# Optimization experiments

Hardware: AMD Instinct MI355X
Metric: run time of the kernel (lower is better)

The kernel has to match this reference:

```python
import jax, jax.numpy as jnp
import numpy as np

B, N, E = 32, 2048, 768
OUT = 384
SPARSITY = 4
LOCAL_C = (E + SPARSITY - 1) // SPARSITY  # 192
HID = 16
LN_EPS = 1e-5


def _layernorm(x, w, b):
    mu = jnp.mean(x, axis=-1, keepdims=True)
    var = jnp.mean(jnp.square(x - mu), axis=-1, keepdims=True)
    return (x - mu) * jax.lax.rsqrt(var + LN_EPS) * w + b


def setup_inputs() -> dict:
    key = jax.random.key(0)
    ks = jax.random.split(key, 8)
    s = 0.02
    return {
        "x": jax.random.normal(ks[0], (B, N, E), dtype=jnp.float32),
        # global head: Linear(E,16) -> LN(16) -> GELU -> Linear(16,1)
        "w_g1": jax.random.normal(ks[1], (E, HID), dtype=jnp.float32) * s,
        "b_g1": jnp.zeros((HID,), dtype=jnp.float32),
        "ln_g_w": jnp.ones((HID,), dtype=jnp.float32),
        "ln_g_b": jnp.zeros((HID,), dtype=jnp.float32),
        "w_g2": jax.random.normal(ks[2], (HID, 1), dtype=jnp.float32) * s,
        "b_g2": jnp.zeros((1,), dtype=jnp.float32),
        # local head: Linear(192,384) -> LN(384) -> GELU
        "w_l": jax.random.normal(ks[3], (LOCAL_C, OUT), dtype=jnp.float32) * s,
        "b_l": jnp.zeros((OUT,), dtype=jnp.float32),
        "ln_l_w": jnp.ones((OUT,), dtype=jnp.float32),
        "ln_l_b": jnp.zeros((OUT,), dtype=jnp.float32),
    }


def reference(x, w_g1, b_g1, ln_g_w, ln_g_b, w_g2, b_g2, w_l, b_l, ln_l_w, ln_l_b):
    # local branch: strided gather -> Linear -> LN -> GELU  [B,N,OUT]
    local = x[..., ::SPARSITY]                                   # [B,N,192]
    local_feat = jax.nn.gelu(_layernorm(local @ w_l + b_l, ln_l_w, ln_l_b),
                             approximate=False)
    # global branch: Linear -> LN -> GELU -> Linear -> [B,N,1] (broadcasts)
    g = jax.nn.gelu(_layernorm(x @ w_g1 + b_g1, ln_g_w, ln_g_b),
                    approximate=False)
    global_feat = g @ w_g2 + b_g2                                # [B,N,1]
    # AdaptiveAvgPool1d(OUT) on last dim; E % OUT == 0 -> exact pairwise mean
    pooled = jnp.mean(x.reshape(B, N, OUT, E // OUT), axis=-1)   # [B,N,OUT]
    return global_feat + pooled + local_feat
```

## Files before the change

### kernel.cpp

```cpp
#include <hip/hip_runtime.h>
#include <hip/hip_bf16.h>

#define B_   32
#define N_   2048
#define E_   768
#define OUT_ 384
#define HID_ 16
constexpr int ROWS   = B_ * N_;
constexpr int TILE_M = 16;
constexpr int NT     = OUT_ / 16;
constexpr int KT_L   = 6;
constexpr int KT_G   = 24;
constexpr int S_AL   = 194;
constexpr int S_PL   = 392;

typedef __attribute__((ext_vector_type(8))) short bf16x8;
typedef __attribute__((ext_vector_type(4))) float f32x4;

__device__ __forceinline__ short f2bf(float f) {
  union { float f; unsigned u; } v; v.f = f;
  unsigned r = v.u + 0x7fffu + ((v.u >> 16) & 1u);
  return (short)(r >> 16);
}
__device__ __forceinline__ float bf2f(short s) {
  union { unsigned u; float f; } v; v.u = ((unsigned)(unsigned short)s) << 16;
  return v.f;
}

__device__ __forceinline__ float fast_erf(float x) {
  const float ax = __builtin_fabsf(x);
  const float t  = __builtin_amdgcn_rcpf(__builtin_fmaf(0.3275911f, ax, 1.0f));
  float p = __builtin_fmaf(1.061405429f, t, -1.453152027f);
  p = __builtin_fmaf(p, t, 1.421413741f);
  p = __builtin_fmaf(p, t, -0.284496736f);
  p = __builtin_fmaf(p, t, 0.254829592f);
  const float e = __expf(-ax * ax);
  const float y = __builtin_fmaf(-p * t, e, 1.0f);
  return __builtin_copysignf(y, x);
}
__device__ __forceinline__ float gelu(float v) {
  return 0.5f * v * (1.0f + fast_erf(v * 0.70710678118654752f));
}

__global__ void prep_kernel(const float* __restrict__ w_l, const float* __restrict__ w_g1,
                            short* __restrict__ wsL, short* __restrict__ wsG) {
  int t = blockIdx.x * blockDim.x + threadIdx.x;
  int wave = t >> 6, ln = t & 63;
  int kg = ln >> 4, c16 = ln & 15;
  if (wave < NT * KT_L) {
    int n = wave / KT_L, ks = wave % KT_L;
    bf16x8 v;
#pragma unroll
    for (int j = 0; j < 8; ++j) {
      int k = ks * 32 + kg * 8 + j;
      v[j] = f2bf(w_l[k * OUT_ + n * 16 + c16]);
    }
    *reinterpret_cast<bf16x8*>(&wsL[(size_t)(wave * 64 + ln) * 8]) = v;
  } else if (wave < NT * KT_L + KT_G) {
    int ks = wave - NT * KT_L;
    bf16x8 v;
#pragma unroll
    for (int j = 0; j < 8; ++j) {
      int k = ks * 32 + kg * 8 + j;
      v[j] = f2bf(w_g1[k * HID_ + c16]);
    }
    *reinterpret_cast<bf16x8*>(&wsG[(size_t)(ks * 64 + ln) * 8]) = v;
  }
}

template <bool USE_WS>
__global__ __launch_bounds__(128, 3)
void spectre_kernel(const float* __restrict__ x,
                    const float* __restrict__ w_g1, const float* __restrict__ b_g1,
                    const float* __restrict__ ln_g_w, const float* __restrict__ ln_g_b,
                    const float* __restrict__ w_g2, const float* __restrict__ b_g2,
                    const float* __restrict__ w_l, const float* __restrict__ b_l,
                    const float* __restrict__ ln_l_w, const float* __restrict__ ln_l_b,
                    const short* __restrict__ wsL, const short* __restrict__ wsG,
                    float* __restrict__ out) {
  __shared__ short al[TILE_M * S_AL];
  __shared__ short pl[TILE_M * S_PL];
  __shared__ float red2[2][16][17];
  __shared__ float reds[2][16][2];

  const int tid = threadIdx.x;
  const int wv  = tid >> 6;
  const int ln  = tid & 63;
  const int kg  = ln >> 4;
  const int l15 = ln & 15;
  const int row0 = blockIdx.x * TILE_M;

  const float* xb = x + (size_t)row0 * E_;

  f32x4 accg = {0.f, 0.f, 0.f, 0.f};
  {
    const float* pA = xb + l15 * E_ + kg * 8;
    float4 xu0[4], xu1[4];
    bf16x8 gb[4];
#pragma unroll
    for (int s = 0; s < 4; ++s) {
      const int ks = wv * 12 + s;
      xu0[s] = *reinterpret_cast<const float4*>(pA + ks * 32);
      xu1[s] = *reinterpret_cast<const float4*>(pA + ks * 32 + 4);
      if constexpr (USE_WS) {
        gb[s] = *reinterpret_cast<const bf16x8*>(&wsG[(ks * 64 + ln) * 8]);
      } else {
#pragma unroll
        for (int j = 0; j < 8; ++j) gb[s][j] = f2bf(w_g1[(ks * 32 + kg * 8 + j) * HID_ + l15]);
      }
    }
#pragma unroll
    for (int i = 0; i < 12; ++i) {
      const int s  = i & 3;
      const int ks = wv * 12 + i;
      const float4 u0 = xu0[s];
      const float4 u1 = xu1[s];
      const bf16x8 b  = gb[s];
      if (i + 4 < 12) {
        const int k2 = ks + 4;
        xu0[s] = *reinterpret_cast<const float4*>(pA + k2 * 32);
        xu1[s] = *reinterpret_cast<const float4*>(pA + k2 * 32 + 4);
        if constexpr (USE_WS) {
          gb[s] = *reinterpret_cast<const bf16x8*>(&wsG[(k2 * 64 + ln) * 8]);
        } else {
#pragma unroll
          for (int j = 0; j < 8; ++j) gb[s][j] = f2bf(w_g1[(k2 * 32 + kg * 8 + j) * HID_ + l15]);
        }
      }
      short2 lv;
      lv.x = f2bf(u0.x);
      lv.y = f2bf(u1.x);
      *reinterpret_cast<short2*>(&al[l15 * S_AL + 8 * ks + 2 * kg]) = lv;
      short4 pv;
      pv.x = f2bf(0.5f * (u0.x + u0.y));
      pv.y = f2bf(0.5f * (u0.z + u0.w));
      pv.z = f2bf(0.5f * (u1.x + u1.y));
      pv.w = f2bf(0.5f * (u1.z + u1.w));
      *reinterpret_cast<short4*>(&pl[l15 * S_PL + ks * 16 + kg * 4]) = pv;
      const bf16x8 a = { lv.x, f2bf(u0.y), f2bf(u0.z), f2bf(u0.w),
                         lv.y, f2bf(u1.y), f2bf(u1.z), f2bf(u1.w) };
      accg = __builtin_amdgcn_mfma_f32_16x16x32_bf16(a, b, accg, 0, 0, 0);
    }
  }
#pragma unroll
  for (int r = 0; r < 4; ++r) red2[wv][kg * 4 + r][l15] = accg[r];

  const float bg  = b_g1[l15];
  const float lgw = ln_g_w[l15];
  const float lgb = ln_g_b[l15];
  const float wg2 = w_g2[l15];
  const float bg2 = b_g2[0];
  float blv[12];
#pragma unroll
  for (int n = 0; n < 12; ++n) blv[n] = b_l[(wv * 12 + n) * 16 + l15];

  __syncthreads();

  f32x4 acc[12];
#pragma unroll
  for (int n = 0; n < 12; ++n) acc[n] = (f32x4){0.f, 0.f, 0.f, 0.f};

  bf16x8 bb[2][6];
#pragma unroll
  for (int j = 0; j < 6; ++j) {
    const int ng = wv * 12 + j;
    if constexpr (USE_WS) {
      bb[0][j] = *reinterpret_cast<const bf16x8*>(&wsL[((ng * KT_L + 0) * 64 + ln) * 8]);
    } else {
#pragma unroll
      for (int jj = 0; jj < 8; ++jj)
        bb[0][j][jj] = f2bf(w_l[(0 * 32 + kg * 8 + jj) * OUT_ + ng * 16 + l15]);
    }
  }
  bf16x8 aLc = *reinterpret_cast<const bf16x8*>(&al[l15 * S_AL + kg * 8]);
  bf16x8 aLn;
#pragma unroll
  for (int ks = 0; ks < KT_L; ++ks) {
#pragma unroll
    for (int j = 0; j < 6; ++j) {
      const int ng = wv * 12 + 6 + j;
      if constexpr (USE_WS) {
        bb[1][j] = *reinterpret_cast<const bf16x8*>(&wsL[((ng * KT_L + ks) * 64 + ln) * 8]);
      } else {
#pragma unroll
        for (int jj = 0; jj < 8; ++jj)
          bb[1][j][jj] = f2bf(w_l[(ks * 32 + kg * 8 + jj) * OUT_ + ng * 16 + l15]);
      }
    }
#pragma unroll
    for (int j = 0; j < 6; ++j)
      acc[j] = __builtin_amdgcn_mfma_f32_16x16x32_bf16(aLc, bb[0][j], acc[j], 0, 0, 0);
    if (ks < KT_L - 1) {
      aLn = *reinterpret_cast<const bf16x8*>(&al[l15 * S_AL + (ks + 1) * 32 + kg * 8]);
#pragma unroll
      for (int j = 0; j < 6; ++j) {
        const int ng = wv * 12 + j;
        if constexpr (USE_WS) {
          bb[0][j] = *reinterpret_cast<const bf16x8*>(&wsL[((ng * KT_L + ks + 1) * 64 + ln) * 8]);
        } else {
#pragma unroll
          for (int jj = 0; jj < 8; ++jj)
            bb[0][j][jj] = f2bf(w_l[((ks + 1) * 32 + kg * 8 + jj) * OUT_ + ng * 16 + l15]);
        }
      }
    }
#pragma unroll
    for (int j = 0; j < 6; ++j)
      acc[6 + j] = __builtin_amdgcn_mfma_f32_16x16x32_bf16(aLc, bb[1][j], acc[6 + j], 0, 0, 0);
    if (ks < KT_L - 1) aLc = aLn;
  }

  float s1[4] = {0.f, 0.f, 0.f, 0.f}, s2[4] = {0.f, 0.f, 0.f, 0.f};
#pragma unroll
  for (int n = 0; n < 12; ++n) {
#pragma unroll
    for (int r = 0; r < 4; ++r) {
      const float v = acc[n][r] + blv[n];
      acc[n][r] = v;
      s1[r] += v;
      s2[r] += v * v;
    }
  }
#pragma unroll
  for (int m = 1; m < 16; m <<= 1) {
#pragma unroll
    for (int r = 0; r < 4; ++r) {
      s1[r] += __shfl_xor(s1[r], m);
      s2[r] += __shfl_xor(s2[r], m);
    }
  }
  if (l15 == 0) {
#pragma unroll
    for (int r = 0; r < 4; ++r) {
      reds[wv][kg * 4 + r][0] = s1[r];
      reds[wv][kg * 4 + r][1] = s2[r];
    }
  }
  __syncthreads();

  float lwv[12], lbv[12];
#pragma unroll
  for (int n = 0; n < 12; ++n) {
    const int col = (wv * 12 + n) * 16 + l15;
    lwv[n] = ln_l_w[col];
    lbv[n] = ln_l_b[col];
  }

  float gf[4];
#pragma unroll
  for (int r = 0; r < 4; ++r) {
    const int row = kg * 4 + r;
    const float y = red2[0][row][l15] + red2[1][row][l15] + bg;
    float s = y, q = y * y;
#pragma unroll
    for (int m = 1; m < 16; m <<= 1) {
      s += __shfl_xor(s, m);
      q += __shfl_xor(q, m);
    }
    const float mean = s * (1.f / 16.f);
    const float var  = q * (1.f / 16.f) - mean * mean;
    const float rstd = rsqrtf(var + 1e-5f);
    const float vn = (y - mean) * rstd * lgw + lgb;
    float ps = gelu(vn) * wg2;
#pragma unroll
    for (int m = 1; m < 16; m <<= 1) ps += __shfl_xor(ps, m);
    gf[r] = ps + bg2;
  }

  float meanr[4], rstdr[4];
#pragma unroll
  for (int r = 0; r < 4; ++r) {
    const int row = kg * 4 + r;
    const float t1 = reds[0][row][0] + reds[1][row][0];
    const float t2 = reds[0][row][1] + reds[1][row][1];
    meanr[r] = t1 * (1.f / 384.f);
    const float var = t2 * (1.f / 384.f) - meanr[r] * meanr[r];
    rstdr[r] = rsqrtf(var + 1e-5f);
  }
#pragma unroll
  for (int n = 0; n < 12; ++n) {
    const int col = (wv * 12 + n) * 16 + l15;
#pragma unroll
    for (int r = 0; r < 4; ++r) {
      const int row = kg * 4 + r;
      const float pooled = bf2f(pl[row * S_PL + col]);
      const float vn = (acc[n][r] - meanr[r]) * rstdr[r] * lwv[n] + lbv[n];
      out[(size_t)(row0 + row) * OUT_ + col] = gelu(vn) + gf[r] + pooled;
    }
  }
}

extern "C" void kernel_launch(void* const* d_in, const int* in_sizes, int n_in,
                              void* d_out, int out_size, void* d_ws, size_t ws_size,
                              hipStream_t stream) {
  (void)in_sizes; (void)n_in; (void)out_size;
  const float* x      = (const float*)d_in[0];
  const float* w_g1   = (const float*)d_in[1];
  const float* b_g1   = (const float*)d_in[2];
  const float* ln_g_w = (const float*)d_in[3];
  const float* ln_g_b = (const float*)d_in[4];
  const float* w_g2   = (const float*)d_in[5];
  const float* b_g2   = (const float*)d_in[6];
  const float* w_l    = (const float*)d_in[7];
  const float* b_l    = (const float*)d_in[8];
  const float* ln_l_w = (const float*)d_in[9];
  const float* ln_l_b = (const float*)d_in[10];
  float* out = (float*)d_out;

  const size_t needL = (size_t)NT * KT_L * 64 * 8;
  const size_t needG = (size_t)KT_G * 64 * 8;
  const bool use_ws = ws_size >= (needL + needG) * sizeof(short);

  short* wsL = (short*)d_ws;
  short* wsG = wsL + needL;

  const int grid = ROWS / TILE_M;
  if (use_ws) {
    prep_kernel<<<(NT * KT_L + KT_G) * 64 / 256, 256, 0, stream>>>(w_l, w_g1, wsL, wsG);
    spectre_kernel<true><<<grid, 128, 0, stream>>>(x, w_g1, b_g1, ln_g_w, ln_g_b, w_g2, b_g2,
                                                   w_l, b_l, ln_l_w, ln_l_b, wsL, wsG, out);
  } else {
    spectre_kernel<false><<<grid, 128, 0, stream>>>(x, w_g1, b_g1, ln_g_w, ln_g_b, w_g2, b_g2,
                                                    w_l, b_l, ln_l_w, ln_l_b, nullptr, nullptr, out);
  }
}
```

Before: 101.4 us.

## Issue all x tile loads up front with inline asm and split-wait consumption

Replaces the rolling 4-deep software prefetch of x and the global-head weights with a scheme that first loads all 12 weight fragments, then issues all 24 x loads as inline-asm global_load_dwordx4 pairs. It waits for the first half with an explicit vmcnt and processes it while the second half is still in flight. It also swaps the hand-written bf16 rounding for the library __float2bfloat16 conversion. The aim is more memory-level parallelism and less compiler-inserted waiting on the load-bound prologue. In exchange it raises register pressure from many live vector registers, and the hand-written waitcnt and sched barriers limit what the compiler can reorder.

Measured after the change: 110.6 us. 9.1% more time.

```diff
diff --git a/kernel.cpp b/kernel.cpp
--- a/kernel.cpp
+++ b/kernel.cpp
@@ -18,13 +18,19 @@
 typedef __attribute__((ext_vector_type(4))) float f32x4;
 
 __device__ __forceinline__ short f2bf(float f) {
-  union { float f; unsigned u; } v; v.f = f;
-  unsigned r = v.u + 0x7fffu + ((v.u >> 16) & 1u);
-  return (short)(r >> 16);
+  __hip_bfloat16 h = __float2bfloat16(f);
+  return __builtin_bit_cast(short, h);
 }
 __device__ __forceinline__ float bf2f(short s) {
   union { unsigned u; float f; } v; v.u = ((unsigned)(unsigned short)s) << 16;
   return v.f;
+}
+
+__device__ __forceinline__ void gload_pair(f32x4& d0, f32x4& d1, const float* a) {
+  asm volatile("global_load_dwordx4 %0, %2, off\n\t"
+               "global_load_dwordx4 %1, %2, off offset:16"
+               : "=&v"(d0), "=&v"(d1)
+               : "v"(a));
 }
 
 __device__ __forceinline__ float fast_erf(float x) {
@@ -93,40 +99,70 @@
   const float* xb = x + (size_t)row0 * E_;
 
   f32x4 accg = {0.f, 0.f, 0.f, 0.f};
-  {
+  if constexpr (USE_WS) {
+    bf16x8 gbv[12];
+#pragma unroll
+    for (int i = 0; i < 12; ++i)
+      gbv[i] = *reinterpret_cast<const bf16x8*>(&wsG[((wv * 12 + i) * 64 + ln) * 8]);
+
+    asm volatile("s_waitcnt vmcnt(0)" ::: "memory");
+    __builtin_amdgcn_sched_barrier(0);
+
+    f32x4 xa0[6], xa1[6], xb0[6], xb1[6];
     const float* pA = xb + l15 * E_ + kg * 8;
-    float4 xu0[4], xu1[4];
-    bf16x8 gb[4];
-#pragma unroll
-    for (int s = 0; s < 4; ++s) {
-      const int ks = wv * 12 + s;
-      xu0[s] = *reinterpret_cast<const float4*>(pA + ks * 32);
-      xu1[s] = *reinterpret_cast<const float4*>(pA + ks * 32 + 4);
-      if constexpr (USE_WS) {
-        gb[s] = *reinterpret_cast<const bf16x8*>(&wsG[(ks * 64 + ln) * 8]);
-      } else {
-#pragma unroll
-        for (int j = 0; j < 8; ++j) gb[s][j] = f2bf(w_g1[(ks * 32 + kg * 8 + j) * HID_ + l15]);
-      }
-    }
+#pragma unroll
+    for (int i = 0; i < 6; ++i) gload_pair(xa0[i], xa1[i], pA + (wv * 12 + i) * 32);
+#pragma unroll
+    for (int i = 0; i < 6; ++i) gload_pair(xb0[i], xb1[i], pA + (wv * 12 + 6 + i) * 32);
+
+    asm volatile("s_waitcnt vmcnt(12)" ::: "memory");
+    __builtin_amdgcn_sched_barrier(0);
+#pragma unroll
+    for (int i = 0; i < 6; ++i) {
+      const int ks = wv * 12 + i;
+      const f32x4 u0 = xa0[i], u1 = xa1[i];
+      short2 lv;
+      lv.x = f2bf(u0[0]);
+      lv.y = f2bf(u1[0]);
+      *reinterpret_cast<short2*>(&al[l15 * S_AL + 8 * ks + 2 * kg]) = lv;
+      short4 pv;
+      pv.x = f2bf(0.5f * (u0[0] + u0[1]));
+      pv.y = f2bf(0.5f * (u0[2] + u0[3]));
+      pv.z = f2bf(0.5f * (u1[0] + u1[1]));
+      pv.w = f2bf(0.5f * (u1[2] + u1[3]));
+      *reinterpret_cast<short4*>(&pl[l15 * S_PL + ks * 16 + kg * 4]) = pv;
+      const bf16x8 a = { lv.x, f2bf(u0[1]), f2bf(u0[2]), f2bf(u0[3]),
+                         lv.y, f2bf(u1[1]), f2bf(u1[2]), f2bf(u1[3]) };
+      accg = __builtin_amdgcn_mfma_f32_16x16x32_bf16(a, gbv[i], accg, 0, 0, 0);
+    }
+    asm volatile("s_waitcnt vmcnt(0)" ::: "memory");
+    __builtin_amdgcn_sched_barrier(0);
+#pragma unroll
+    for (int i = 0; i < 6; ++i) {
+      const int ks = wv * 12 + 6 + i;
+      const f32x4 u0 = xb0[i], u1 = xb1[i];
+      short2 lv;
+      lv.x = f2bf(u0[0]);
+      lv.y = f2bf(u1[0]);
+      *reinterpret_cast<short2*>(&al[l15 * S_AL + 8 * ks + 2 * kg]) = lv;
+      short4 pv;
+      pv.x = f2bf(0.5f * (u0[0] + u0[1]));
+      pv.y = f2bf(0.5f * (u0[2] + u0[3]));
+      pv.z = f2bf(0.5f * (u1[0] + u1[1]));
+      pv.w = f2bf(0.5f * (u1[2] + u1[3]));
+      *reinterpret_cast<short4*>(&pl[l15 * S_PL + ks * 16 + kg * 4]) = pv;
+      const bf16x8 a = { lv.x, f2bf(u0[1]), f2bf(u0[2]), f2bf(u0[3]),
+                         lv.y, f2bf(u1[1]), f2bf(u1[2]), f2bf(u1[3]) };
+      accg = __builtin_amdgcn_mfma_f32_16x16x32_bf16(a, gbv[6 + i], accg, 0, 0, 0);
+    }
+    __builtin_amdgcn_sched_barrier(0);
+  } else {
+    const float* pA = xb + l15 * E_ + kg * 8;
 #pragma unroll
     for (int i = 0; i < 12; ++i) {
-      const int s  = i & 3;
       const int ks = wv * 12 + i;
-      const float4 u0 = xu0[s];
-      const float4 u1 = xu1[s];
-      const bf16x8 b  = gb[s];
-      if (i + 4 < 12) {
-        const int k2 = ks + 4;
-        xu0[s] = *reinterpret_cast<const float4*>(pA + k2 * 32);
-        xu1[s] = *reinterpret_cast<const float4*>(pA + k2 * 32 + 4);
-        if constexpr (USE_WS) {
-          gb[s] = *reinterpret_cast<const bf16x8*>(&wsG[(k2 * 64 + ln) * 8]);
-        } else {
-#pragma unroll
-          for (int j = 0; j < 8; ++j) gb[s][j] = f2bf(w_g1[(k2 * 32 + kg * 8 + j) * HID_ + l15]);
-        }
-      }
+      const float4 u0 = *reinterpret_cast<const float4*>(pA + ks * 32);
+      const float4 u1 = *reinterpret_cast<const float4*>(pA + ks * 32 + 4);
       short2 lv;
       lv.x = f2bf(u0.x);
       lv.y = f2bf(u1.x);
@@ -137,6 +173,9 @@
       pv.z = f2bf(0.5f * (u1.x + u1.y));
       pv.w = f2bf(0.5f * (u1.z + u1.w));
       *reinterpret_cast<short4*>(&pl[l15 * S_PL + ks * 16 + kg * 4]) = pv;
+      bf16x8 b;
+#pragma unroll
+      for (int j = 0; j < 8; ++j) b[j] = f2bf(w_g1[(ks * 32 + kg * 8 + j) * HID_ + l15]);
       const bf16x8 a = { lv.x, f2bf(u0.y), f2bf(u0.z), f2bf(u0.w),
                          lv.y, f2bf(u1.y), f2bf(u1.z), f2bf(u1.w) };
       accg = __builtin_amdgcn_mfma_f32_16x16x32_bf16(a, b, accg, 0, 0, 0);
```
